# Kernel tuning notes

Hardware: AMD Instinct MI355X
Metric: run time of the kernel (lower is better)

## Reference

```python
import jax, jax.numpy as jnp
import numpy as np
import math

D_MODEL = 1024
D_STATE = 64
DT_MIN = 0.001
DT_MAX = 0.1
BATCH = 4
SEQLEN = 4096


def make_hippo_matrix(N):
    P = np.sqrt(1 + 2 * np.arange(N))
    A = P[:, np.newaxis] * P[np.newaxis, :]
    A = np.tril(A) - np.diag(np.arange(N))
    return jnp.asarray(-A, dtype=jnp.float32)


def setup_inputs() -> dict:
    key = jax.random.key(0)
    k_u, k_B, k_C, k_D, k_dt = jax.random.split(key, 5)
    u = jax.random.normal(k_u, (BATCH, SEQLEN, D_MODEL), dtype=jnp.float32)
    A = make_hippo_matrix(D_STATE)  # (N, N) HiPPO-LegS buffer
    B = jax.random.normal(k_B, (D_STATE, 1), dtype=jnp.float32)
    C = jax.random.normal(k_C, (1, D_STATE), dtype=jnp.float32)
    D = jax.random.normal(k_D, (1,), dtype=jnp.float32)
    log_dt = (jax.random.uniform(k_dt, (1,), dtype=jnp.float32)
              * (math.log(DT_MAX) - math.log(DT_MIN)) + math.log(DT_MIN))
    return {"u": u, "A": A, "B": B, "C": C, "D": D, "log_dt": log_dt}


def _forward(u, A, B, C, D, log_dt):
    n = A.shape[0]
    dt = jnp.exp(log_dt)[0]
    A_bar = jax.scipy.linalg.expm(dt * A)                     # (N, N)
    B_bar = jnp.linalg.solve(A, (A_bar - jnp.eye(n, dtype=A.dtype)) @ B)  # (N, 1)
    bvec = B_bar[:, 0]          # (N,)
    cvec = C[0]                 # (N,)
    d_scalar = D[0]
    # Faithful to source: only channel 0 of u drives the SSM.
    u0 = u[:, :, 0]             # (Bn, L)

    def step(x, u_t):
        # x: (Bn, N), u_t: (Bn,)
        x = x @ A_bar.T + u_t[:, None] * bvec
        y = x @ cvec + d_scalar * u_t   # (Bn,)
        return x, y

    x0 = jnp.zeros((u.shape[0], n), dtype=u.dtype)
    _, ys = jax.lax.scan(step, x0, jnp.swapaxes(u0, 0, 1))   # (L, Bn)
    # Scalar output broadcast across all H channels (matches torch expand)
    y = jnp.broadcast_to(jnp.swapaxes(ys, 0, 1)[:, :, None], u.shape)
    return y


def reference(u, A, B, C, D, log_dt):
    return _forward(u, A, B, C, D, log_dt)
```

## Files before the change

### kernel.cpp

```cpp
#include <hip/hip_runtime.h>


#define NT 256
#define MP 68
#define MB (64 * MP)

typedef __attribute__((ext_vector_type(8))) short v8s;
typedef __attribute__((ext_vector_type(4))) float v4f;

__device__ __forceinline__ unsigned short bf16r(float x) {
  union { float f; unsigned u; } v; v.f = x;
  unsigned r = v.u + 0x7fffu + ((v.u >> 16) & 1u);
  return (unsigned short)(r >> 16);
}
__device__ __forceinline__ float bf2f(unsigned short h) {
  union { unsigned u; float f; } v; v.u = ((unsigned)h) << 16;
  return v.f;
}
__device__ __forceinline__ void cvt4(const float4 f, ushort4* H, ushort4* L) {
  unsigned short h;
  h = bf16r(f.x); H->x = h; L->x = bf16r(f.x - bf2f(h));
  h = bf16r(f.y); H->y = h; L->y = bf16r(f.y - bf2f(h));
  h = bf16r(f.z); H->z = h; L->z = bf16r(f.z - bf2f(h));
  h = bf16r(f.w); H->w = h; L->w = bf16r(f.w - bf2f(h));
}

__device__ void mm(const float* Ag, const float* Bs, int bT,
                   float* Cd, int cpitch, float* Cd2,
                   int nrt, int nct, int rowbase, int colbase,
                   unsigned short* FRAG) {
  const int t = threadIdx.x;
  __syncthreads();
  for (int s0 = 0; s0 < 512; s0 += 256) {
    const int s = s0 + t;
    const int l = s & 63, Tq = s >> 6;
    const int mrow = (Tq >> 1) * 16 + (l & 15);
    const int kk = (Tq & 1) * 32 + (l >> 4) * 8;
    const float* ap = Ag + mrow * MP + kk;
    const float4 f0 = *(const float4*)ap;
    const float4 f1 = *(const float4*)(ap + 4);
    ushort4 H0, L0, H1, L1;
    cvt4(f0, &H0, &L0); cvt4(f1, &H1, &L1);
    *(ushort4*)(FRAG + s * 8)            = H0;
    *(ushort4*)(FRAG + s * 8 + 4)        = H1;
    *(ushort4*)(FRAG + 4096 + s * 8)     = L0;
    *(ushort4*)(FRAG + 4096 + s * 8 + 4) = L1;
    float4 g0, g1;
    if (bT) {
      const float* bp = Bs + mrow * MP + kk;
      g0 = *(const float4*)bp;
      g1 = *(const float4*)(bp + 4);
    } else {
      g0.x = Bs[(kk + 0) * MP + mrow]; g0.y = Bs[(kk + 1) * MP + mrow];
      g0.z = Bs[(kk + 2) * MP + mrow]; g0.w = Bs[(kk + 3) * MP + mrow];
      g1.x = Bs[(kk + 4) * MP + mrow]; g1.y = Bs[(kk + 5) * MP + mrow];
      g1.z = Bs[(kk + 6) * MP + mrow]; g1.w = Bs[(kk + 7) * MP + mrow];
    }
    cvt4(g0, &H0, &L0); cvt4(g1, &H1, &L1);
    *(ushort4*)(FRAG + 8192 + s * 8)      = H0;
    *(ushort4*)(FRAG + 8192 + s * 8 + 4)  = H1;
    *(ushort4*)(FRAG + 12288 + s * 8)     = L0;
    *(ushort4*)(FRAG + 12288 + s * 8 + 4) = L1;
  }
  __syncthreads();
  {
    const int w = t >> 6, l = t & 63;
    if (w < nrt) {
      const v8s Ah0 = *(const v8s*)(FRAG + ((w * 2 + 0) * 64 + l) * 8);
      const v8s Ah1 = *(const v8s*)(FRAG + ((w * 2 + 1) * 64 + l) * 8);
      const v8s Al0 = *(const v8s*)(FRAG + 4096 + ((w * 2 + 0) * 64 + l) * 8);
      const v8s Al1 = *(const v8s*)(FRAG + 4096 + ((w * 2 + 1) * 64 + l) * 8);
      for (int Cc = 0; Cc < nct; ++Cc) {
        const v8s Bh0 = *(const v8s*)(FRAG + 8192 + ((Cc * 2 + 0) * 64 + l) * 8);
        const v8s Bh1 = *(const v8s*)(FRAG + 8192 + ((Cc * 2 + 1) * 64 + l) * 8);
        const v8s Bl0 = *(const v8s*)(FRAG + 12288 + ((Cc * 2 + 0) * 64 + l) * 8);
        const v8s Bl1 = *(const v8s*)(FRAG + 12288 + ((Cc * 2 + 1) * 64 + l) * 8);
        const v4f z = {0.f, 0.f, 0.f, 0.f};
        v4f a0 = __builtin_amdgcn_mfma_f32_16x16x32_bf16(Ah0, Bh0, z, 0, 0, 0);
        a0 = __builtin_amdgcn_mfma_f32_16x16x32_bf16(Ah1, Bh1, a0, 0, 0, 0);
        v4f a1 = __builtin_amdgcn_mfma_f32_16x16x32_bf16(Ah0, Bl0, z, 0, 0, 0);
        a1 = __builtin_amdgcn_mfma_f32_16x16x32_bf16(Ah1, Bl1, a1, 0, 0, 0);
        v4f a2 = __builtin_amdgcn_mfma_f32_16x16x32_bf16(Al0, Bh0, z, 0, 0, 0);
        a2 = __builtin_amdgcn_mfma_f32_16x16x32_bf16(Al1, Bh1, a2, 0, 0, 0);
        const int col = colbase + Cc * 16 + (l & 15);
        const int r0 = rowbase + w * 16 + (l >> 4) * 4;
        const float o0 = a0[0] + a1[0] + a2[0];
        const float o1 = a0[1] + a1[1] + a2[1];
        const float o2 = a0[2] + a1[2] + a2[2];
        const float o3 = a0[3] + a1[3] + a2[3];
        Cd[(r0 + 0) * cpitch + col] = o0;
        Cd[(r0 + 1) * cpitch + col] = o1;
        Cd[(r0 + 2) * cpitch + col] = o2;
        Cd[(r0 + 3) * cpitch + col] = o3;
        if (Cd2) {
          Cd2[(r0 + 0) * MP + col] = o0;
          Cd2[(r0 + 1) * MP + col] = o1;
          Cd2[(r0 + 2) * MP + col] = o2;
          Cd2[(r0 + 3) * MP + col] = o3;
        }
      }
    }
  }
  __syncthreads();
}

__device__ __forceinline__ void mv64row(const float* M, const float* vin,
                                        float* vout, float* out2, int half) {
  const int t = threadIdx.x;
  __syncthreads();
  const int w = t >> 6, l = t & 63;
  const int row = w * 16 + (l >> 2), q = l & 3;
  const float* mp = M + row * MP + q * 16;
  const float* vp = vin + q * 16;
  float p = 0.f;
#pragma unroll
  for (int j = 0; j < 16; j += 4) {
    const float4 m = *(const float4*)(mp + j);
    p = fmaf(m.x, vp[j + 0], p);
    p = fmaf(m.y, vp[j + 1], p);
    p = fmaf(m.z, vp[j + 2], p);
    p = fmaf(m.w, vp[j + 3], p);
  }
  p += __shfl_xor(p, 1);
  p += __shfl_xor(p, 2);
  if (q == 0) {
    float s = half ? 0.5f * (p + vin[row]) : p;
    vout[row] = s;
    if (out2) out2[row] = s;
  }
  __syncthreads();
}

__device__ __forceinline__ void mv64colT(const float* M, const float* vin,
                                         float* vout, float* out2) {
  const int t = threadIdx.x;
  __syncthreads();
  const int w = t >> 6, l = t & 63;
  const int col = w * 16 + (l >> 2), q = l & 3;
  float p = 0.f;
#pragma unroll
  for (int j = 0; j < 16; ++j)
    p = fmaf(M[(q * 16 + j) * MP + col], vin[q * 16 + j], p);
  p += __shfl_xor(p, 1);
  p += __shfl_xor(p, 2);
  if (q == 0) {
    vout[col] = p;
    if (out2) out2[col] = p;
  }
  __syncthreads();
}

__device__ void buildG(float* dst, const float* X, const float* X2, const float* X3,
                       float c0, float c1, float c2, float c3, const float* addsrc) {
  const int t = threadIdx.x;
  __syncthreads();
  const int r = t >> 2, cb = (t & 3) * 16;
#pragma unroll
  for (int j = 0; j < 16; j += 4) {
    const int c = cb + j;
    const int e = r * MP + c;
    const float4 x1 = *(const float4*)(X + e);
    const float4 x2 = *(const float4*)(X2 + e);
    const float4 x3 = *(const float4*)(X3 + e);
    float4 v;
    v.x = fmaf(c1, x1.x, fmaf(c2, x2.x, c3 * x3.x));
    v.y = fmaf(c1, x1.y, fmaf(c2, x2.y, c3 * x3.y));
    v.z = fmaf(c1, x1.z, fmaf(c2, x2.z, c3 * x3.z));
    v.w = fmaf(c1, x1.w, fmaf(c2, x2.w, c3 * x3.w));
    if (r == c + 0) v.x += c0;
    if (r == c + 1) v.y += c0;
    if (r == c + 2) v.z += c0;
    if (r == c + 3) v.w += c0;
    if (addsrc) {
      const float4 a = *(const float4*)(addsrc + e);
      v.x += a.x; v.y += a.y; v.z += a.z; v.w += a.w;
    }
    *(float4*)(dst + e) = v;
  }
  __syncthreads();
}

__global__ __launch_bounds__(NT) void s4_setup(const float* __restrict__ u,
    const float* __restrict__ A, const float* __restrict__ Bv,
    const float* __restrict__ Cv, const float* __restrict__ logdt,
    float* __restrict__ ws) {
  if (blockIdx.x > 0) {
    const int idx = (blockIdx.x - 1) * NT + threadIdx.x;
    ws[4096 + idx] = u[(size_t)idx * 1024];
    return;
  }
  __shared__ __align__(16) float S0[MB];
  __shared__ __align__(16) float SX[MB];
  __shared__ __align__(16) float SX2[MB];
  __shared__ __align__(16) float SX3[MB];
  __shared__ __align__(16) float SU0[MB];
  __shared__ __align__(16) float SU1[MB];
  __shared__ __align__(16) unsigned short FRAG[16384];
  __shared__ float vB[64], v1[64], v2[64], v3[64], va[64], vb[64], vg[64];
  __shared__ int s_s;
  float* vscr = (float*)FRAG;

  const int t = threadIdx.x;
  float* kbuf = ws;
  float* SBRT = SU0;
  float* SCQT = SU1;
  const float dt = expf(logdt[0]);

  const float invf[17] = {1.f, 1.f, 1.f / 2.f, 1.f / 6.f, 1.f / 24.f, 1.f / 120.f,
                          1.f / 720.f, 1.f / 5040.f, 1.f / 40320.f, 1.f / 362880.f,
                          1.f / 3628800.f, 1.f / 39916800.f, 1.f / 479001600.f,
                          1.f / 6.2270208e9f, 1.f / 8.71782912e10f,
                          1.f / 1.307674368e12f, 1.f / 2.0922789888e13f};

  {
    const int j = t & 63, w = t >> 6;
    float p = 0.f;
#pragma unroll
    for (int ii = 0; ii < 16; ++ii) p += fabsf(A[(w * 16 + ii) * 64 + j]);
    vscr[t] = p;
    __syncthreads();
    if (t < 64) {
      float cs = vscr[t] + vscr[64 + t] + vscr[128 + t] + vscr[192 + t];
      cs *= dt;
#pragma unroll
      for (int off = 32; off > 0; off >>= 1) cs = fmaxf(cs, __shfl_xor(cs, off));
      if (t == 0) {
        int s = 0;
        while (cs > 2.0f && s < 30) { cs *= 0.5f; ++s; }
        s_s = s;
      }
    }
    __syncthreads();
  }
  const int sq = s_s;
  const float scl = ldexpf(dt, -sq);

  {
    const int r = t >> 2, cb = (t & 3) * 16;
#pragma unroll
    for (int j = 0; j < 16; j += 4) {
      const float4 a4 = *(const float4*)(A + r * 64 + cb + j);
      float4 x;
      x.x = a4.x * scl; x.y = a4.y * scl; x.z = a4.z * scl; x.w = a4.w * scl;
      *(float4*)(S0 + r * MP + cb + j) = x;
      *(float4*)(SX + r * MP + cb + j) = x;
    }
    if (t < 64) vB[t] = Bv[t];
    __syncthreads();
  }

  mm(S0, S0, 0, S0, MP, SX2, 4, 4, 0, 0, FRAG);
  mm(SX, S0, 0, SX3, MP, nullptr, 4, 4, 0, 0, FRAG);
  mm(S0, S0, 0, S0, MP, nullptr, 4, 4, 0, 0, FRAG);

  mv64row(SX,  vB, v1, nullptr, 0);
  mv64row(SX2, vB, v2, nullptr, 0);
  mv64row(SX3, vB, v3, nullptr, 0);
  if (t < 64)
    va[t] = invf[13] * vB[t] + invf[14] * v1[t] + invf[15] * v2[t] + invf[16] * v3[t];
  __syncthreads();
  mv64row(S0, va, vb, nullptr, 0);
  if (t < 64)
    va[t] = invf[9] * vB[t] + invf[10] * v1[t] + invf[11] * v2[t] + invf[12] * v3[t] + vb[t];
  __syncthreads();
  mv64row(S0, va, vb, nullptr, 0);
  if (t < 64)
    va[t] = invf[5] * vB[t] + invf[6] * v1[t] + invf[7] * v2[t] + invf[8] * v3[t] + vb[t];
  __syncthreads();
  mv64row(S0, va, vb, nullptr, 0);
  if (t < 64)
    vg[t] = invf[1] * vB[t] + invf[2] * v1[t] + invf[3] * v2[t] + invf[4] * v3[t] + vb[t];
  __syncthreads();

  buildG(SU0, SX, SX2, SX3, invf[12], invf[13], invf[14], invf[15], nullptr);
  mm(SU0, S0, 0, SU1, MP, nullptr, 4, 4, 0, 0, FRAG);
  buildG(SU1, SX, SX2, SX3, invf[8], invf[9], invf[10], invf[11], SU1);
  mm(SU1, S0, 0, SU0, MP, nullptr, 4, 4, 0, 0, FRAG);
  buildG(SU0, SX, SX2, SX3, invf[4], invf[5], invf[6], invf[7], SU0);
  mm(SU0, S0, 0, S0, MP, nullptr, 4, 4, 0, 0, FRAG);
  buildG(S0, SX, SX2, SX3, invf[0], invf[1], invf[2], invf[3], S0);

  float* vcur = vg;
  float* vnxt = va;
  for (int it = 0; it < sq; ++it) {
    mv64row(S0, vcur, vnxt, nullptr, 1);
    { float* tmp = vcur; vcur = vnxt; vnxt = tmp; }
    mm(S0, S0, 0, S0, MP, nullptr, 4, 4, 0, 0, FRAG);
  }

  if (t < 64) {
    const float bb = dt * vcur[t];
    v1[t] = bb;
    SBRT[t] = bb;
  }
  __syncthreads();
  {
    float* vc = v1; float* vn = v2;
    for (int r = 1; r < 16; ++r) {
      mv64row(S0, vc, vn, SBRT + r * MP, 0);
      float* tmp = vc; vc = vn; vn = tmp;
    }
  }

  mm(S0, S0, 0, S0, MP, nullptr, 4, 4, 0, 0, FRAG);
  mm(S0, S0, 0, S0, MP, nullptr, 4, 4, 0, 0, FRAG);
  mm(S0, S0, 0, S0, MP, nullptr, 4, 4, 0, 0, FRAG);
  mm(S0, S0, 0, S0, MP, nullptr, 4, 4, 0, 0, FRAG);
  mm(SBRT, S0, 1, SBRT, MP, nullptr, 1, 4, 16, 0, FRAG);
  mm(S0, S0, 0, S0, MP, nullptr, 4, 4, 0, 0, FRAG);
  mm(SBRT, S0, 1, SBRT, MP, nullptr, 2, 4, 32, 0, FRAG);
  mm(S0, S0, 0, S0, MP, nullptr, 4, 4, 0, 0, FRAG);

  if (t < 64) {
    const float cc = Cv[t];
    v1[t] = cc;
    SCQT[t] = cc;
  }
  __syncthreads();
  {
    float* vc = v1; float* vn = v2;
    for (int qx = 1; qx < 16; ++qx) {
      mv64colT(S0, vc, vn, SCQT + qx * MP);
      float* tmp = vc; vc = vn; vn = tmp;
    }
  }

  mm(S0, S0, 0, S0, MP, nullptr, 4, 4, 0, 0, FRAG);
  mm(S0, S0, 0, S0, MP, nullptr, 4, 4, 0, 0, FRAG);
  mm(S0, S0, 0, S0, MP, nullptr, 4, 4, 0, 0, FRAG);
  mm(S0, S0, 0, S0, MP, nullptr, 4, 4, 0, 0, FRAG);
  mm(SCQT, S0, 0, SCQT, MP, nullptr, 1, 4, 16, 0, FRAG);
  mm(S0, S0, 0, S0, MP, nullptr, 4, 4, 0, 0, FRAG);
  mm(SCQT, S0, 0, SCQT, MP, nullptr, 2, 4, 32, 0, FRAG);

  mm(SCQT, SBRT, 1, kbuf, 64, nullptr, 4, 4, 0, 0, FRAG);
}

__global__ __launch_bounds__(256) void s4_out(const float* __restrict__ ws,
                                              const float* __restrict__ Dp,
                                              float* __restrict__ out) {
  const int bid = blockIdx.x;
  const int b = bid >> 10;
  const int t0 = (bid & 1023) << 2;
  const float* kb = ws;
  const float* ub = ws + 4096 + (b << 12);
  const int tid = threadIdx.x;

  float a0 = 0.f, a1 = 0.f, a2 = 0.f, a3 = 0.f;
  for (int s0 = tid << 2; s0 <= t0; s0 += 1024) {
    const float4 uv = *(const float4*)(ub + s0);
    const int b0 = t0 - s0;
    const float4 k0 = *(const float4*)(kb + b0);
    float4 k1 = make_float4(0.f, 0.f, 0.f, 0.f);
    if (b0 >= 4) k1 = *(const float4*)(kb + b0 - 4);
    a0 = fmaf(k0.x, uv.x, a0);
    a0 = fmaf(k1.w, uv.y, a0);
    a0 = fmaf(k1.z, uv.z, a0);
    a0 = fmaf(k1.y, uv.w, a0);
    a1 = fmaf(k0.y, uv.x, a1);
    a1 = fmaf(k0.x, uv.y, a1);
    a1 = fmaf(k1.w, uv.z, a1);
    a1 = fmaf(k1.z, uv.w, a1);
    a2 = fmaf(k0.z, uv.x, a2);
    a2 = fmaf(k0.y, uv.y, a2);
    a2 = fmaf(k0.x, uv.z, a2);
    a2 = fmaf(k1.w, uv.w, a2);
    a3 = fmaf(k0.w, uv.x, a3);
    a3 = fmaf(k0.z, uv.y, a3);
    a3 = fmaf(k0.y, uv.z, a3);
    a3 = fmaf(k0.x, uv.w, a3);
  }
#pragma unroll
  for (int off = 32; off > 0; off >>= 1) {
    a0 += __shfl_xor(a0, off);
    a1 += __shfl_xor(a1, off);
    a2 += __shfl_xor(a2, off);
    a3 += __shfl_xor(a3, off);
  }
  __shared__ float red[4][4];
  __shared__ float sy[4];
  if ((tid & 63) == 0) {
    const int w = tid >> 6;
    red[0][w] = a0; red[1][w] = a1; red[2][w] = a2; red[3][w] = a3;
  }
  __syncthreads();
  if (tid < 4)
    sy[tid] = red[tid][0] + red[tid][1] + red[tid][2] + red[tid][3] +
              Dp[0] * ub[t0 + tid];
  __syncthreads();
  const int row = tid >> 6, lx = tid & 63;
  const float y = sy[row];
  const v4f y4 = {y, y, y, y};
  v4f* dst = (v4f*)(out + ((size_t)(b << 12) + t0 + row) * 1024);
  __builtin_nontemporal_store(y4, dst + lx);
  __builtin_nontemporal_store(y4, dst + lx + 64);
  __builtin_nontemporal_store(y4, dst + lx + 128);
  __builtin_nontemporal_store(y4, dst + lx + 192);
}

extern "C" void kernel_launch(void* const* d_in, const int* in_sizes, int n_in,
                              void* d_out, int out_size, void* d_ws, size_t ws_size,
                              hipStream_t stream) {
  const float* u  = (const float*)d_in[0];
  const float* A  = (const float*)d_in[1];
  const float* B  = (const float*)d_in[2];
  const float* C  = (const float*)d_in[3];
  const float* D  = (const float*)d_in[4];
  const float* ld = (const float*)d_in[5];
  float* ws = (float*)d_ws;

  s4_setup<<<65, NT, 0, stream>>>(u, A, B, C, ld, ws);
  s4_out<<<4096, 256, 0, stream>>>(ws, D, (float*)d_out);
}
```

Measured before the change: 177.8 us.

## Fuse Padé matrix building into MFMA matmul and load A fragments directly

The 64x64 split-bf16 MFMA matmul helper becomes a template. Each wave now builds its A fragments straight from the fp32 source in shared memory instead of staging them through the FRAG buffer, which halves FRAG. The separate buildG passes that form the polynomial matrix terms are folded into the A-load prologue and the C-store epilogue. The vector Horner steps are also fused into the matrix-vector kernel. Together these cut barriers and shared-memory round trips in the single-block setup kernel, at the cost of redundant A loads across column tiles and more register pressure.

```diff
diff --git a/kernel.cpp b/kernel.cpp
--- a/kernel.cpp
+++ b/kernel.cpp
@@ -24,79 +24,114 @@
   h = bf16r(f.z); H->z = h; L->z = bf16r(f.z - bf2f(h));
   h = bf16r(f.w); H->w = h; L->w = bf16r(f.w - bf2f(h));
 }
-
-__device__ void mm(const float* Ag, const float* Bs, int bT,
-                   float* Cd, int cpitch, float* Cd2,
-                   int nrt, int nct, int rowbase, int colbase,
-                   unsigned short* FRAG) {
+__device__ __forceinline__ void cvt8(const float4 f0, const float4 f1,
+                                     v8s* H, v8s* L) {
+  union { v8s v; ushort4 u[2]; } Hu, Lu;
+  cvt4(f0, &Hu.u[0], &Lu.u[0]);
+  cvt4(f1, &Hu.u[1], &Lu.u[1]);
+  *H = Hu.v; *L = Lu.v;
+}
+
+template<int NRT, int NCT, int BT, int FA, int FC>
+__device__ void mm(const float* Ag, const float* Bs, float* Cd, int cpitch,
+                   float* Cd2, int rowbase,
+                   const float* GX, const float* GX2, const float* GX3,
+                   float4 cA, float4 cC, unsigned short* FRAG) {
   const int t = threadIdx.x;
   __syncthreads();
+#pragma unroll
   for (int s0 = 0; s0 < 512; s0 += 256) {
     const int s = s0 + t;
     const int l = s & 63, Tq = s >> 6;
-    const int mrow = (Tq >> 1) * 16 + (l & 15);
+    const int col = (Tq >> 1) * 16 + (l & 15);
     const int kk = (Tq & 1) * 32 + (l >> 4) * 8;
-    const float* ap = Ag + mrow * MP + kk;
-    const float4 f0 = *(const float4*)ap;
-    const float4 f1 = *(const float4*)(ap + 4);
+    float4 g0, g1;
+    if (BT) {
+      const float* bp = Bs + col * MP + kk;
+      g0 = *(const float4*)bp;
+      g1 = *(const float4*)(bp + 4);
+    } else {
+      g0.x = Bs[(kk + 0) * MP + col]; g0.y = Bs[(kk + 1) * MP + col];
+      g0.z = Bs[(kk + 2) * MP + col]; g0.w = Bs[(kk + 3) * MP + col];
+      g1.x = Bs[(kk + 4) * MP + col]; g1.y = Bs[(kk + 5) * MP + col];
+      g1.z = Bs[(kk + 6) * MP + col]; g1.w = Bs[(kk + 7) * MP + col];
+    }
     ushort4 H0, L0, H1, L1;
-    cvt4(f0, &H0, &L0); cvt4(f1, &H1, &L1);
+    cvt4(g0, &H0, &L0); cvt4(g1, &H1, &L1);
     *(ushort4*)(FRAG + s * 8)            = H0;
     *(ushort4*)(FRAG + s * 8 + 4)        = H1;
     *(ushort4*)(FRAG + 4096 + s * 8)     = L0;
     *(ushort4*)(FRAG + 4096 + s * 8 + 4) = L1;
-    float4 g0, g1;
-    if (bT) {
-      const float* bp = Bs + mrow * MP + kk;
-      g0 = *(const float4*)bp;
-      g1 = *(const float4*)(bp + 4);
-    } else {
-      g0.x = Bs[(kk + 0) * MP + mrow]; g0.y = Bs[(kk + 1) * MP + mrow];
-      g0.z = Bs[(kk + 2) * MP + mrow]; g0.w = Bs[(kk + 3) * MP + mrow];
-      g1.x = Bs[(kk + 4) * MP + mrow]; g1.y = Bs[(kk + 5) * MP + mrow];
-      g1.z = Bs[(kk + 6) * MP + mrow]; g1.w = Bs[(kk + 7) * MP + mrow];
-    }
-    cvt4(g0, &H0, &L0); cvt4(g1, &H1, &L1);
-    *(ushort4*)(FRAG + 8192 + s * 8)      = H0;
-    *(ushort4*)(FRAG + 8192 + s * 8 + 4)  = H1;
-    *(ushort4*)(FRAG + 12288 + s * 8)     = L0;
-    *(ushort4*)(FRAG + 12288 + s * 8 + 4) = L1;
   }
   __syncthreads();
   {
     const int w = t >> 6, l = t & 63;
-    if (w < nrt) {
-      const v8s Ah0 = *(const v8s*)(FRAG + ((w * 2 + 0) * 64 + l) * 8);
-      const v8s Ah1 = *(const v8s*)(FRAG + ((w * 2 + 1) * 64 + l) * 8);
-      const v8s Al0 = *(const v8s*)(FRAG + 4096 + ((w * 2 + 0) * 64 + l) * 8);
-      const v8s Al1 = *(const v8s*)(FRAG + 4096 + ((w * 2 + 1) * 64 + l) * 8);
-      for (int Cc = 0; Cc < nct; ++Cc) {
-        const v8s Bh0 = *(const v8s*)(FRAG + 8192 + ((Cc * 2 + 0) * 64 + l) * 8);
-        const v8s Bh1 = *(const v8s*)(FRAG + 8192 + ((Cc * 2 + 1) * 64 + l) * 8);
-        const v8s Bl0 = *(const v8s*)(FRAG + 12288 + ((Cc * 2 + 0) * 64 + l) * 8);
-        const v8s Bl1 = *(const v8s*)(FRAG + 12288 + ((Cc * 2 + 1) * 64 + l) * 8);
+    if (w < NRT) {
+      const int m = l & 15, g = l >> 4;
+      v8s Ah[2], Al[2];
+#pragma unroll
+      for (int h = 0; h < 2; ++h) {
+        const int row = w * 16 + m;
+        const int kb = h * 32 + g * 8;
+        const int e = row * MP + kb;
+        float4 f0, f1;
+        if (FA) {
+          const float4 x0 = *(const float4*)(GX + e);
+          const float4 x1 = *(const float4*)(GX + e + 4);
+          const float4 y0 = *(const float4*)(GX2 + e);
+          const float4 y1 = *(const float4*)(GX2 + e + 4);
+          const float4 z0 = *(const float4*)(GX3 + e);
+          const float4 z1 = *(const float4*)(GX3 + e + 4);
+          f0.x = fmaf(cA.y, x0.x, fmaf(cA.z, y0.x, cA.w * z0.x));
+          f0.y = fmaf(cA.y, x0.y, fmaf(cA.z, y0.y, cA.w * z0.y));
+          f0.z = fmaf(cA.y, x0.z, fmaf(cA.z, y0.z, cA.w * z0.z));
+          f0.w = fmaf(cA.y, x0.w, fmaf(cA.z, y0.w, cA.w * z0.w));
+          f1.x = fmaf(cA.y, x1.x, fmaf(cA.z, y1.x, cA.w * z1.x));
+          f1.y = fmaf(cA.y, x1.y, fmaf(cA.z, y1.y, cA.w * z1.y));
+          f1.z = fmaf(cA.y, x1.z, fmaf(cA.z, y1.z, cA.w * z1.z));
+          f1.w = fmaf(cA.y, x1.w, fmaf(cA.z, y1.w, cA.w * z1.w));
+          if (row == kb + 0) f0.x += cA.x;
+          if (row == kb + 1) f0.y += cA.x;
+          if (row == kb + 2) f0.z += cA.x;
+          if (row == kb + 3) f0.w += cA.x;
+          if (row == kb + 4) f1.x += cA.x;
+          if (row == kb + 5) f1.y += cA.x;
+          if (row == kb + 6) f1.z += cA.x;
+          if (row == kb + 7) f1.w += cA.x;
+        } else {
+          f0 = *(const float4*)(Ag + e);
+          f1 = *(const float4*)(Ag + e + 4);
+        }
+        cvt8(f0, f1, &Ah[h], &Al[h]);
+      }
+#pragma unroll
+      for (int Cc = 0; Cc < NCT; ++Cc) {
+        const v8s Bh0 = *(const v8s*)(FRAG + ((Cc * 2 + 0) * 64 + l) * 8);
+        const v8s Bh1 = *(const v8s*)(FRAG + ((Cc * 2 + 1) * 64 + l) * 8);
+        const v8s Bl0 = *(const v8s*)(FRAG + 4096 + ((Cc * 2 + 0) * 64 + l) * 8);
+        const v8s Bl1 = *(const v8s*)(FRAG + 4096 + ((Cc * 2 + 1) * 64 + l) * 8);
         const v4f z = {0.f, 0.f, 0.f, 0.f};
-        v4f a0 = __builtin_amdgcn_mfma_f32_16x16x32_bf16(Ah0, Bh0, z, 0, 0, 0);
-        a0 = __builtin_amdgcn_mfma_f32_16x16x32_bf16(Ah1, Bh1, a0, 0, 0, 0);
-        v4f a1 = __builtin_amdgcn_mfma_f32_16x16x32_bf16(Ah0, Bl0, z, 0, 0, 0);
-        a1 = __builtin_amdgcn_mfma_f32_16x16x32_bf16(Ah1, Bl1, a1, 0, 0, 0);
-        v4f a2 = __builtin_amdgcn_mfma_f32_16x16x32_bf16(Al0, Bh0, z, 0, 0, 0);
-        a2 = __builtin_amdgcn_mfma_f32_16x16x32_bf16(Al1, Bh1, a2, 0, 0, 0);
-        const int col = colbase + Cc * 16 + (l & 15);
-        const int r0 = rowbase + w * 16 + (l >> 4) * 4;
-        const float o0 = a0[0] + a1[0] + a2[0];
-        const float o1 = a0[1] + a1[1] + a2[1];
-        const float o2 = a0[2] + a1[2] + a2[2];
-        const float o3 = a0[3] + a1[3] + a2[3];
-        Cd[(r0 + 0) * cpitch + col] = o0;
-        Cd[(r0 + 1) * cpitch + col] = o1;
-        Cd[(r0 + 2) * cpitch + col] = o2;
-        Cd[(r0 + 3) * cpitch + col] = o3;
-        if (Cd2) {
-          Cd2[(r0 + 0) * MP + col] = o0;
-          Cd2[(r0 + 1) * MP + col] = o1;
-          Cd2[(r0 + 2) * MP + col] = o2;
-          Cd2[(r0 + 3) * MP + col] = o3;
+        v4f a0 = __builtin_amdgcn_mfma_f32_16x16x32_bf16(Ah[0], Bh0, z, 0, 0, 0);
+        a0 = __builtin_amdgcn_mfma_f32_16x16x32_bf16(Ah[1], Bh1, a0, 0, 0, 0);
+        v4f a1 = __builtin_amdgcn_mfma_f32_16x16x32_bf16(Ah[0], Bl0, z, 0, 0, 0);
+        a1 = __builtin_amdgcn_mfma_f32_16x16x32_bf16(Ah[1], Bl1, a1, 0, 0, 0);
+        v4f a2 = __builtin_amdgcn_mfma_f32_16x16x32_bf16(Al[0], Bh0, z, 0, 0, 0);
+        a2 = __builtin_amdgcn_mfma_f32_16x16x32_bf16(Al[1], Bh1, a2, 0, 0, 0);
+        const int col = Cc * 16 + m;
+        const int r0 = rowbase + w * 16 + g * 4;
+#pragma unroll
+        for (int i = 0; i < 4; ++i) {
+          float o = a0[i] + a1[i] + a2[i];
+          if (FC) {
+            const int rr = w * 16 + g * 4 + i;
+            const int eg = rr * MP + col;
+            o = fmaf(cC.y, GX[eg], o);
+            o = fmaf(cC.z, GX2[eg], o);
+            o = fmaf(cC.w, GX3[eg], o);
+            if (rr == col) o += cC.x;
+          }
+          Cd[(r0 + i) * cpitch + col] = o;
+          if (Cd2) Cd2[(r0 + i) * MP + col] = o;
         }
       }
     }
@@ -128,6 +163,32 @@
     vout[row] = s;
     if (out2) out2[row] = s;
   }
+  __syncthreads();
+}
+
+__device__ __forceinline__ void mv64row_phi(const float* M, const float* vin,
+    float* vout, const float* vB, const float* v1, const float* v2,
+    const float* v3, float4 pc) {
+  const int t = threadIdx.x;
+  __syncthreads();
+  const int w = t >> 6, l = t & 63;
+  const int row = w * 16 + (l >> 2), q = l & 3;
+  const float* mp = M + row * MP + q * 16;
+  const float* vp = vin + q * 16;
+  float p = 0.f;
+#pragma unroll
+  for (int j = 0; j < 16; j += 4) {
+    const float4 m = *(const float4*)(mp + j);
+    p = fmaf(m.x, vp[j + 0], p);
+    p = fmaf(m.y, vp[j + 1], p);
+    p = fmaf(m.z, vp[j + 2], p);
+    p = fmaf(m.w, vp[j + 3], p);
+  }
+  p += __shfl_xor(p, 1);
+  p += __shfl_xor(p, 2);
+  if (q == 0)
+    vout[row] = fmaf(pc.x, vB[row], fmaf(pc.y, v1[row],
+                fmaf(pc.z, v2[row], fmaf(pc.w, v3[row], p))));
   __syncthreads();
 }
 
@@ -146,36 +207,6 @@
   if (q == 0) {
     vout[col] = p;
     if (out2) out2[col] = p;
-  }
-  __syncthreads();
-}
-
-__device__ void buildG(float* dst, const float* X, const float* X2, const float* X3,
-                       float c0, float c1, float c2, float c3, const float* addsrc) {
-  const int t = threadIdx.x;
-  __syncthreads();
-  const int r = t >> 2, cb = (t & 3) * 16;
-#pragma unroll
-  for (int j = 0; j < 16; j += 4) {
-    const int c = cb + j;
-    const int e = r * MP + c;
-    const float4 x1 = *(const float4*)(X + e);
-    const float4 x2 = *(const float4*)(X2 + e);
-    const float4 x3 = *(const float4*)(X3 + e);
-    float4 v;
-    v.x = fmaf(c1, x1.x, fmaf(c2, x2.x, c3 * x3.x));
-    v.y = fmaf(c1, x1.y, fmaf(c2, x2.y, c3 * x3.y));
-    v.z = fmaf(c1, x1.z, fmaf(c2, x2.z, c3 * x3.z));
-    v.w = fmaf(c1, x1.w, fmaf(c2, x2.w, c3 * x3.w));
-    if (r == c + 0) v.x += c0;
-    if (r == c + 1) v.y += c0;
-    if (r == c + 2) v.z += c0;
-    if (r == c + 3) v.w += c0;
-    if (addsrc) {
-      const float4 a = *(const float4*)(addsrc + e);
-      v.x += a.x; v.y += a.y; v.z += a.z; v.w += a.w;
-    }
-    *(float4*)(dst + e) = v;
   }
   __syncthreads();
 }
@@ -195,7 +226,7 @@
   __shared__ __align__(16) float SX3[MB];
   __shared__ __align__(16) float SU0[MB];
   __shared__ __align__(16) float SU1[MB];
-  __shared__ __align__(16) unsigned short FRAG[16384];
+  __shared__ __align__(16) unsigned short FRAG[8192];
   __shared__ float vB[64], v1[64], v2[64], v3[64], va[64], vb[64], vg[64];
   __shared__ int s_s;
   float* vscr = (float*)FRAG;
@@ -205,6 +236,7 @@
   float* SBRT = SU0;
   float* SCQT = SU1;
   const float dt = expf(logdt[0]);
+  const float4 zf4 = make_float4(0.f, 0.f, 0.f, 0.f);
 
   const float invf[17] = {1.f, 1.f, 1.f / 2.f, 1.f / 6.f, 1.f / 24.f, 1.f / 120.f,
                           1.f / 720.f, 1.f / 5040.f, 1.f / 40320.f, 1.f / 362880.f,
@@ -249,9 +281,9 @@
     __syncthreads();
   }
 
-  mm(S0, S0, 0, S0, MP, SX2, 4, 4, 0, 0, FRAG);
-  mm(SX, S0, 0, SX3, MP, nullptr, 4, 4, 0, 0, FRAG);
-  mm(S0, S0, 0, S0, MP, nullptr, 4, 4, 0, 0, FRAG);
+  mm<4,4,0,0,0>(S0, S0, S0, MP, SX2, 0, SX, SX2, SX3, zf4, zf4, FRAG);
+  mm<4,4,0,0,0>(SX, S0, SX3, MP, nullptr, 0, SX, SX2, SX3, zf4, zf4, FRAG);
+  mm<4,4,0,0,0>(S0, S0, S0, MP, nullptr, 0, SX, SX2, SX3, zf4, zf4, FRAG);
 
   mv64row(SX,  vB, v1, nullptr, 0);
   mv64row(SX2, vB, v2, nullptr, 0);
@@ -259,33 +291,27 @@
   if (t < 64)
     va[t] = invf[13] * vB[t] + invf[14] * v1[t] + invf[15] * v2[t] + invf[16] * v3[t];
   __syncthreads();
-  mv64row(S0, va, vb, nullptr, 0);
-  if (t < 64)
-    va[t] = invf[9] * vB[t] + invf[10] * v1[t] + invf[11] * v2[t] + invf[12] * v3[t] + vb[t];
-  __syncthreads();
-  mv64row(S0, va, vb, nullptr, 0);
-  if (t < 64)
-    va[t] = invf[5] * vB[t] + invf[6] * v1[t] + invf[7] * v2[t] + invf[8] * v3[t] + vb[t];
-  __syncthreads();
-  mv64row(S0, va, vb, nullptr, 0);
-  if (t < 64)
-    vg[t] = invf[1] * vB[t] + invf[2] * v1[t] + invf[3] * v2[t] + invf[4] * v3[t] + vb[t];
-  __syncthreads();
-
-  buildG(SU0, SX, SX2, SX3, invf[12], invf[13], invf[14], invf[15], nullptr);
-  mm(SU0, S0, 0, SU1, MP, nullptr, 4, 4, 0, 0, FRAG);
-  buildG(SU1, SX, SX2, SX3, invf[8], invf[9], invf[10], invf[11], SU1);
-  mm(SU1, S0, 0, SU0, MP, nullptr, 4, 4, 0, 0, FRAG);
-  buildG(SU0, SX, SX2, SX3, invf[4], invf[5], invf[6], invf[7], SU0);
-  mm(SU0, S0, 0, S0, MP, nullptr, 4, 4, 0, 0, FRAG);
-  buildG(S0, SX, SX2, SX3, invf[0], invf[1], invf[2], invf[3], S0);
+  mv64row_phi(S0, va, vb, vB, v1, v2, v3,
+              make_float4(invf[9], invf[10], invf[11], invf[12]));
+  mv64row_phi(S0, vb, va, vB, v1, v2, v3,
+              make_float4(invf[5], invf[6], invf[7], invf[8]));
+  mv64row_phi(S0, va, vg, vB, v1, v2, v3,
+              make_float4(invf[1], invf[2], invf[3], invf[4]));
+
+  mm<4,4,0,1,1>(nullptr, S0, SU1, MP, nullptr, 0, SX, SX2, SX3,
+                make_float4(invf[12], invf[13], invf[14], invf[15]),
+                make_float4(invf[8], invf[9], invf[10], invf[11]), FRAG);
+  mm<4,4,0,0,1>(SU1, S0, SU0, MP, nullptr, 0, SX, SX2, SX3, zf4,
+                make_float4(invf[4], invf[5], invf[6], invf[7]), FRAG);
+  mm<4,4,0,0,1>(SU0, S0, S0, MP, nullptr, 0, SX, SX2, SX3, zf4,
+                make_float4(invf[0], invf[1], invf[2], invf[3]), FRAG);
 
   float* vcur = vg;
   float* vnxt = va;
   for (int it = 0; it < sq; ++it) {
     mv64row(S0, vcur, vnxt, nullptr, 1);
     { float* tmp = vcur; vcur = vnxt; vnxt = tmp; }
-    mm(S0, S0, 0, S0, MP, nullptr, 4, 4, 0, 0, FRAG);
+    mm<4,4,0,0,0>(S0, S0, S0, MP, nullptr, 0, SX, SX2, SX3, zf4, zf4, FRAG);
   }
 
   if (t < 64) {
@@ -302,14 +328,14 @@
     }
   }
 
-  mm(S0, S0, 0, S0, MP, nullptr, 4, 4, 0, 0, FRAG);
-  mm(S0, S0, 0, S0, MP, nullptr, 4, 4, 0, 0, FRAG);
-  mm(S0, S0, 0, S0, MP, nullptr, 4, 4, 0, 0, FRAG);
-  mm(S0, S0, 0, S0, MP, nullptr, 4, 4, 0, 0, FRAG);
-  mm(SBRT, S0, 1, SBRT, MP, nullptr, 1, 4, 16, 0, FRAG);
-  mm(S0, S0, 0, S0, MP, nullptr, 4, 4, 0, 0, FRAG);
-  mm(SBRT, S0, 1, SBRT, MP, nullptr, 2, 4, 32, 0, FRAG);
-  mm(S0, S0, 0, S0, MP, nullptr, 4, 4, 0, 0, FRAG);
+  mm<4,4,0,0,0>(S0, S0, S0, MP, nullptr, 0, SX, SX2, SX3, zf4, zf4, FRAG);
+  mm<4,4,0,0,0>(S0, S0, S0, MP, nullptr, 0, SX, SX2, SX3, zf4, zf4, FRAG);
+  mm<4,4,0,0,0>(S0, S0, S0, MP, nullptr, 0, SX, SX2, SX3, zf4, zf4, FRAG);
+  mm<4,4,0,0,0>(S0, S0, S0, MP, nullptr, 0, SX, SX2, SX3, zf4, zf4, FRAG);
+  mm<1,4,1,0,0>(SBRT, S0, SBRT, MP, nullptr, 16, SX, SX2, SX3, zf4, zf4, FRAG);
+  mm<4,4,0,0,0>(S0, S0, S0, MP, nullptr, 0, SX, SX2, SX3, zf4, zf4, FRAG);
+  mm<2,4,1,0,0>(SBRT, S0, SBRT, MP, nullptr, 32, SX, SX2, SX3, zf4, zf4, FRAG);
+  mm<4,4,0,0,0>(S0, S0, S0, MP, nullptr, 0, SX, SX2, SX3, zf4, zf4, FRAG);
 
   if (t < 64) {
     const float cc = Cv[t];
@@ -325,15 +351,15 @@
     }
   }
 
-  mm(S0, S0, 0, S0, MP, nullptr, 4, 4, 0, 0, FRAG);
-  mm(S0, S0, 0, S0, MP, nullptr, 4, 4, 0, 0, FRAG);
-  mm(S0, S0, 0, S0, MP, nullptr, 4, 4, 0, 0, FRAG);
-  mm(S0, S0, 0, S0, MP, nullptr, 4, 4, 0, 0, FRAG);
-  mm(SCQT, S0, 0, SCQT, MP, nullptr, 1, 4, 16, 0, FRAG);
-  mm(S0, S0, 0, S0, MP, nullptr, 4, 4, 0, 0, FRAG);
-  mm(SCQT, S0, 0, SCQT, MP, nullptr, 2, 4, 32, 0, FRAG);
-
-  mm(SCQT, SBRT, 1, kbuf, 64, nullptr, 4, 4, 0, 0, FRAG);
+  mm<4,4,0,0,0>(S0, S0, S0, MP, nullptr, 0, SX, SX2, SX3, zf4, zf4, FRAG);
+  mm<4,4,0,0,0>(S0, S0, S0, MP, nullptr, 0, SX, SX2, SX3, zf4, zf4, FRAG);
+  mm<4,4,0,0,0>(S0, S0, S0, MP, nullptr, 0, SX, SX2, SX3, zf4, zf4, FRAG);
+  mm<4,4,0,0,0>(S0, S0, S0, MP, nullptr, 0, SX, SX2, SX3, zf4, zf4, FRAG);
+  mm<1,4,0,0,0>(SCQT, S0, SCQT, MP, nullptr, 16, SX, SX2, SX3, zf4, zf4, FRAG);
+  mm<4,4,0,0,0>(S0, S0, S0, MP, nullptr, 0, SX, SX2, SX3, zf4, zf4, FRAG);
+  mm<2,4,0,0,0>(SCQT, S0, SCQT, MP, nullptr, 32, SX, SX2, SX3, zf4, zf4, FRAG);
+
+  mm<4,4,1,0,0>(SCQT, SBRT, kbuf, 64, nullptr, 0, SX, SX2, SX3, zf4, zf4, FRAG);
 }
 
 __global__ __launch_bounds__(256) void s4_out(const float* __restrict__ ws,
```

After: 170.8 us. -3.9%, faster.
